# Optimization experiments

Measured on AMD Instinct MI355X. Metric: run time of the kernel, lower is better.

Reference implementation:

```python
import jax, jax.numpy as jnp
import numpy as np

SCALE = 1.0  # std of the Normal error model (init arg `scale`)
B, P, D, T = 32, 256, 64, 4096


def setup_inputs() -> dict:
    key = jax.random.key(0)
    k1, k2, k3 = jax.random.split(key, 3)
    data = jax.random.normal(k1, (B, P, D), dtype=jnp.float32)
    targets = jax.random.normal(k2, (B, P), dtype=jnp.float32)
    task_pool = jax.random.normal(k3, (T, D, 1), dtype=jnp.float32)
    return {"data": data, "targets": targets, "task_pool": task_pool}


def reference(data, targets, task_pool):
    # W: (n_dims, n_tasks), matching task_pool.squeeze(-1).T in the original
    W = task_pool[..., 0].T
    dt = data.dtype

    # Per-point, per-task predictions and Gaussian log-likelihoods, computed ONCE.
    # The original recomputes X@W and the log-prob sum for every prefix i (O(n^2));
    # here a single cumsum over the point axis reproduces the same prefix sums.
    pred_per_task = jnp.einsum('bpd,dt->bpt', data, W)          # (B, P, T)
    err = targets[..., None] - pred_per_task                     # (B, P, T)
    log_norm = -jnp.log(jnp.asarray(SCALE, dt)) - 0.5 * jnp.log(jnp.asarray(2.0 * np.pi, dt))
    scores = -0.5 * (err / SCALE) ** 2 + log_norm                # Normal(0, scale).log_prob

    cum = jnp.cumsum(scores, axis=1)                             # cum[:, i] = sum_{j<=i}
    # Posterior for predicting point i uses points 0..i-1; point 0 uses a uniform
    # posterior (original: W.mean(dim=1) == softmax(zeros) @ W.T).
    log_lik = jnp.concatenate([jnp.zeros_like(cum[:, :1]), cum[:, :-1]], axis=1)
    post = jax.nn.softmax(log_lik, axis=-1)                      # (B, P, T)

    w_mmse = jnp.einsum('bpt,dt->bpd', post, W)                  # posterior-mean weights
    return jnp.einsum('bpd,bpd->bp', data, w_mmse)               # (B, P)
```

## Files before the change

kernel.cpp:

```cpp
#include <hip/hip_runtime.h>
#include <hip/hip_bf16.h>
#include <math.h>

#define Bb 32
#define Pp 256
#define Dd 64
#define Tt 4096

typedef unsigned short ushort_t;
typedef __attribute__((ext_vector_type(8))) short bf16x8;
typedef __attribute__((ext_vector_type(4))) float f32x4;

#define TRIP_BYTES ((size_t)Bb * Pp * 64 * 16)
#define A_BF_BYTES ((size_t)Bb * Pp * Dd * 2)
#define B_BF_BYTES ((size_t)Tt * Dd * 2)
#define WS_NEED    (TRIP_BYTES + 2 * A_BF_BYTES + 2 * B_BF_BYTES)

#define MFMA6(a)                                                     \
  a = __builtin_amdgcn_mfma_f32_16x16x32_bf16(ah0, bh0, a, 0, 0, 0); \
  a = __builtin_amdgcn_mfma_f32_16x16x32_bf16(ah1, bh1, a, 0, 0, 0); \
  a = __builtin_amdgcn_mfma_f32_16x16x32_bf16(ah0, bl0, a, 0, 0, 0); \
  a = __builtin_amdgcn_mfma_f32_16x16x32_bf16(al0, bh0, a, 0, 0, 0); \
  a = __builtin_amdgcn_mfma_f32_16x16x32_bf16(ah1, bl1, a, 0, 0, 0); \
  a = __builtin_amdgcn_mfma_f32_16x16x32_bf16(al1, bh1, a, 0, 0, 0);

__global__ __launch_bounds__(256) void k_conv(const float* __restrict__ data,
                                              const float* __restrict__ Wt,
                                              ushort_t* __restrict__ Ah, ushort_t* __restrict__ Al,
                                              ushort_t* __restrict__ Bh, ushort_t* __restrict__ Bl) {
  const int i  = blockIdx.x * 256 + threadIdx.x;
  const int NA = Bb * Pp * Dd;
  const float x = (i < NA) ? data[i] : Wt[i - NA];
  const __hip_bfloat16 h = __float2bfloat16(x);
  const float hf = __bfloat162float(h);
  const __hip_bfloat16 l = __float2bfloat16(x - hf);
  if (i < NA) { Ah[i] = *(const ushort_t*)&h; Al[i] = *(const ushort_t*)&l; }
  else        { const int j = i - NA;
                Bh[j] = *(const ushort_t*)&h; Bl[j] = *(const ushort_t*)&l; }
}

__global__ __launch_bounds__(256, 2) void k_main(const ushort_t* __restrict__ Ah,
                                                 const ushort_t* __restrict__ Al,
                                                 const ushort_t* __restrict__ Bh,
                                                 const ushort_t* __restrict__ Bl,
                                                 const float* __restrict__ targets,
                                                 float4* __restrict__ triples) {
  __shared__ short Bhs[256 * 72];
  __shared__ short Bls[256 * 72];
  const int tid  = threadIdx.x;
  const int wid  = tid >> 6;
  const int lane = tid & 63;
  const int quad = lane >> 4;
  const int l16  = lane & 15;
  const int b     = blockIdx.x >> 4;
  const int strip = blockIdx.x & 15;
  const int t0    = strip * 256;

  {
    const float4* sh = (const float4*)(Bh + (size_t)t0 * Dd);
    const float4* sl = (const float4*)(Bl + (size_t)t0 * Dd);
#pragma unroll
    for (int j = 0; j < 8; ++j) {
      const int idx = tid + j * 256;
      const int tl  = idx >> 3;
      const int col = (idx & 7) * 8;
      *(float4*)&Bhs[tl * 72 + col] = sh[idx];
      *(float4*)&Bls[tl * 72 + col] = sl[idx];
    }
  }
  __syncthreads();

  const ushort_t* arow_base = Ah + (size_t)b * Pp * Dd;
  const ushort_t* alow_base = Al + (size_t)b * Pp * Dd;
  float4* __restrict__ trb  = triples + (size_t)b * Pp * 64;
  const int wstrip = strip * 4 + wid;

  float R[4];
#pragma unroll
  for (int nt = 0; nt < 4; ++nt) R[nt] = 0.f;

#pragma unroll 1
  for (int sg = 0; sg < 16; ++sg) {
    const int p0 = sg * 16;
    const size_t aoff = (size_t)(p0 + l16) * Dd + quad * 8;
    const bf16x8 ah0 = *(const bf16x8*)(arow_base + aoff);
    const bf16x8 ah1 = *(const bf16x8*)(arow_base + aoff + 32);
    const bf16x8 al0 = *(const bf16x8*)(alow_base + aoff);
    const bf16x8 al1 = *(const bf16x8*)(alow_base + aoff + 32);
    const float4 tq  = *(const float4*)(targets + b * Pp + p0 + quad * 4);

    float cc[4][4], av[4][4];
#pragma unroll
    for (int nt = 0; nt < 4; ++nt) {
      const int tl = wid * 64 + nt * 16 + l16;
      const int bo = tl * 72 + quad * 8;
      const bf16x8 bh0 = *(const bf16x8*)&Bhs[bo];
      const bf16x8 bh1 = *(const bf16x8*)&Bhs[bo + 32];
      const bf16x8 bl0 = *(const bf16x8*)&Bls[bo];
      const bf16x8 bl1 = *(const bf16x8*)&Bls[bo + 32];
      f32x4 a = (f32x4)0.f;
      MFMA6(a)

      float sc[4];
      { const float e = tq.x - a[0]; sc[0] = -0.5f * e * e; }
      { const float e = tq.y - a[1]; sc[1] = -0.5f * e * e; }
      { const float e = tq.z - a[2]; sc[2] = -0.5f * e * e; }
      { const float e = tq.w - a[3]; sc[3] = -0.5f * e * e; }

      const float colsum = (sc[0] + sc[1]) + (sc[2] + sc[3]);
      const float x1 = __shfl_xor(colsum, 16, 64);
      const float x2 = __shfl_xor(colsum, 32, 64);
      const float x3 = __shfl_xor(x1, 32, 64);
      const float pre = (quad == 0) ? 0.f
                      : (quad == 1) ? x1
                      : (quad == 2) ? (x2 + x3)
                                    : (x1 + x2 + x3);
      const float base = R[nt] + pre;
      cc[nt][0] = base;
      cc[nt][1] = base + sc[0];
      cc[nt][2] = cc[nt][1] + sc[1];
      cc[nt][3] = cc[nt][2] + sc[2];
#pragma unroll
      for (int r = 0; r < 4; ++r) av[nt][r] = a[r];

      R[nt] += ((colsum + x1) + (x2 + x3));
    }

    float mm[4], ss[4], vv[4];
#pragma unroll
    for (int r = 0; r < 4; ++r) {
      const float m01 = fmaxf(cc[0][r], cc[1][r]);
      const float m23 = fmaxf(cc[2][r], cc[3][r]);
      mm[r] = fmaxf(m01, m23);
      float s = 0.f, v = 0.f;
#pragma unroll
      for (int nt = 0; nt < 4; ++nt) {
        const float e = __expf(cc[nt][r] - mm[r]);
        s += e;
        v = fmaf(e, av[nt][r], v);
      }
      ss[r] = s; vv[r] = v;
    }

    float M[4];
#pragma unroll
    for (int r = 0; r < 4; ++r) M[r] = mm[r];
#pragma unroll
    for (int off = 1; off < 16; off <<= 1)
#pragma unroll
      for (int r = 0; r < 4; ++r) M[r] = fmaxf(M[r], __shfl_xor(M[r], off, 64));
#pragma unroll
    for (int r = 0; r < 4; ++r) {
      const float f = __expf(mm[r] - M[r]);
      ss[r] *= f; vv[r] *= f;
    }
#pragma unroll
    for (int off = 1; off < 16; off <<= 1)
#pragma unroll
      for (int r = 0; r < 4; ++r) {
        ss[r] += __shfl_xor(ss[r], off, 64);
        vv[r] += __shfl_xor(vv[r], off, 64);
      }

    if (l16 == 0) {
#pragma unroll
      for (int r = 0; r < 4; ++r) {
        const int p = p0 + quad * 4 + r;
        trb[p * 64 + wstrip] = make_float4(M[r], ss[r], vv[r], 0.f);
      }
    }
  }
}

__global__ __launch_bounds__(256) void k_merge(const float4* __restrict__ ws,
                                               float* __restrict__ out) {
  const int gt   = blockIdx.x * 256 + threadIdx.x;
  const int bp   = gt >> 6;
  const int lane = gt & 63;
  const float4 o = ws[(size_t)bp * 64 + lane];
  const float m = o.x, s = o.y, v = o.z;
  float M = m;
#pragma unroll
  for (int off = 32; off; off >>= 1) M = fmaxf(M, __shfl_xor(M, off, 64));
  const float f = __expf(m - M);
  float S = f * s, V = f * v;
#pragma unroll
  for (int off = 32; off; off >>= 1) {
    S += __shfl_xor(S, off, 64);
    V += __shfl_xor(V, off, 64);
  }
  if (lane == 0) out[bp] = V / S;
}

__global__ __launch_bounds__(256) void k_scan_fused(const float* __restrict__ data,
                                                    const float* __restrict__ targets,
                                                    const float* __restrict__ task_pool,
                                                    float4* __restrict__ ws) {
  const int b     = blockIdx.x >> 4;
  const int wid   = threadIdx.x >> 6;
  const int lane  = threadIdx.x & 63;
  const int chunk = ((blockIdx.x & 15) << 2) | wid;
  const int t     = (chunk << 6) | lane;
  float w[Dd];
#pragma unroll
  for (int d = 0; d < Dd; d += 4) {
    const float4 r = *(const float4*)(task_pool + (size_t)t * Dd + d);
    w[d] = r.x; w[d + 1] = r.y; w[d + 2] = r.z; w[d + 3] = r.w;
  }
  const float* drow = data + (size_t)b * (Pp * Dd);
  const float* tgt  = targets + b * Pp;
  float4* wsb       = ws + (size_t)b * (Pp * 64);
  float c = 0.f;
  for (int p = 0; p < Pp; ++p) {
    float a0 = 0.f, a1 = 0.f, a2 = 0.f, a3 = 0.f;
    const float* r = drow + p * Dd;
#pragma unroll
    for (int d = 0; d < Dd; d += 4) {
      a0 = fmaf(r[d], w[d], a0);         a1 = fmaf(r[d + 1], w[d + 1], a1);
      a2 = fmaf(r[d + 2], w[d + 2], a2); a3 = fmaf(r[d + 3], w[d + 3], a3);
    }
    const float pred = (a0 + a1) + (a2 + a3);
    float m = c;
#pragma unroll
    for (int off = 32; off; off >>= 1) m = fmaxf(m, __shfl_xor(m, off, 64));
    const float e = __expf(c - m);
    float s = e, v = e * pred;
#pragma unroll
    for (int off = 32; off; off >>= 1) {
      s += __shfl_xor(s, off, 64);
      v += __shfl_xor(v, off, 64);
    }
    if (lane == 0) wsb[p * 64 + chunk] = make_float4(m, s, v, 0.f);
    const float err = tgt[p] - pred;
    c = fmaf(-0.5f * err, err, c);
  }
}

extern "C" void kernel_launch(void* const* d_in, const int* in_sizes, int n_in,
                              void* d_out, int out_size, void* d_ws, size_t ws_size,
                              hipStream_t stream) {
  const float* data      = (const float*)d_in[0];
  const float* targets   = (const float*)d_in[1];
  const float* task_pool = (const float*)d_in[2];
  float* out = (float*)d_out;

  if (ws_size >= WS_NEED) {
    float4*   trips = (float4*)d_ws;
    char*     cb    = (char*)d_ws + TRIP_BYTES;
    ushort_t* Ah    = (ushort_t*)cb;
    ushort_t* Al    = (ushort_t*)(cb + A_BF_BYTES);
    ushort_t* Bh    = (ushort_t*)(cb + 2 * A_BF_BYTES);
    ushort_t* Bl    = (ushort_t*)(cb + 2 * A_BF_BYTES + B_BF_BYTES);
    k_conv <<<dim3((Bb * Pp * Dd + Tt * Dd) / 256), dim3(256), 0, stream>>>(
        data, task_pool, Ah, Al, Bh, Bl);
    k_main <<<dim3(Bb * 16), dim3(256), 0, stream>>>(Ah, Al, Bh, Bl, targets, trips);
    k_merge<<<dim3((Bb * Pp * 64) / 256), dim3(256), 0, stream>>>(trips, out);
  } else {
    float4* triples = (float4*)d_ws;
    k_scan_fused<<<dim3(512), dim3(256), 0, stream>>>(data, targets, task_pool, triples);
    k_merge<<<dim3((Bb * Pp * 64) / 256), dim3(256), 0, stream>>>(triples, out);
  }
}
```

Before: 104.6 us.

## Fuse bf16 split conversion into main kernel and halve task strip width

Removes the separate conversion kernel by splitting fp32 data and task weights into bf16 hi/lo pairs inside the main MFMA kernel. Each block now covers 128 tasks instead of 256, which doubles the grid and allows four blocks per CU. The number of partial softmax triples per point doubles to 128, so the merge kernel reads two triples per lane and does a pairwise online-softmax butterfly. The cost is redundant on-the-fly conversion of the data rows across task strips and more intermediate traffic.

```diff
diff --git a/kernel.cpp b/kernel.cpp
--- a/kernel.cpp
+++ b/kernel.cpp
@@ -11,10 +11,20 @@
 typedef __attribute__((ext_vector_type(8))) short bf16x8;
 typedef __attribute__((ext_vector_type(4))) float f32x4;
 
-#define TRIP_BYTES ((size_t)Bb * Pp * 64 * 16)
-#define A_BF_BYTES ((size_t)Bb * Pp * Dd * 2)
-#define B_BF_BYTES ((size_t)Tt * Dd * 2)
-#define WS_NEED    (TRIP_BYTES + 2 * A_BF_BYTES + 2 * B_BF_BYTES)
+#define TRIP2_BYTES ((size_t)Bb * Pp * 128 * 16)
+#define TRIP_BYTES  ((size_t)Bb * Pp * 64 * 16)
+
+__device__ __forceinline__ void split8(const float* __restrict__ x,
+                                       bf16x8& hi, bf16x8& lo) {
+#pragma unroll
+  for (int j = 0; j < 8; ++j) {
+    const __hip_bfloat16 hb = __float2bfloat16(x[j]);
+    const float hf = __bfloat162float(hb);
+    const __hip_bfloat16 lb = __float2bfloat16(x[j] - hf);
+    hi[j] = *(const short*)&hb;
+    lo[j] = *(const short*)&lb;
+  }
+}
 
 #define MFMA6(a)                                                     \
   a = __builtin_amdgcn_mfma_f32_16x16x32_bf16(ah0, bh0, a, 0, 0, 0); \
@@ -24,75 +34,72 @@
   a = __builtin_amdgcn_mfma_f32_16x16x32_bf16(ah1, bl1, a, 0, 0, 0); \
   a = __builtin_amdgcn_mfma_f32_16x16x32_bf16(al1, bh1, a, 0, 0, 0);
 
-__global__ __launch_bounds__(256) void k_conv(const float* __restrict__ data,
-                                              const float* __restrict__ Wt,
-                                              ushort_t* __restrict__ Ah, ushort_t* __restrict__ Al,
-                                              ushort_t* __restrict__ Bh, ushort_t* __restrict__ Bl) {
-  const int i  = blockIdx.x * 256 + threadIdx.x;
-  const int NA = Bb * Pp * Dd;
-  const float x = (i < NA) ? data[i] : Wt[i - NA];
-  const __hip_bfloat16 h = __float2bfloat16(x);
-  const float hf = __bfloat162float(h);
-  const __hip_bfloat16 l = __float2bfloat16(x - hf);
-  if (i < NA) { Ah[i] = *(const ushort_t*)&h; Al[i] = *(const ushort_t*)&l; }
-  else        { const int j = i - NA;
-                Bh[j] = *(const ushort_t*)&h; Bl[j] = *(const ushort_t*)&l; }
-}
-
-__global__ __launch_bounds__(256, 2) void k_main(const ushort_t* __restrict__ Ah,
-                                                 const ushort_t* __restrict__ Al,
-                                                 const ushort_t* __restrict__ Bh,
-                                                 const ushort_t* __restrict__ Bl,
-                                                 const float* __restrict__ targets,
-                                                 float4* __restrict__ triples) {
-  __shared__ short Bhs[256 * 72];
-  __shared__ short Bls[256 * 72];
+__global__ __launch_bounds__(256, 4) void k_main2(const float* __restrict__ data,
+                                                  const float* __restrict__ Wt,
+                                                  const float* __restrict__ targets,
+                                                  float4* __restrict__ triples) {
+  __shared__ short Bhs[128 * 72];
+  __shared__ short Bls[128 * 72];
   const int tid  = threadIdx.x;
   const int wid  = tid >> 6;
   const int lane = tid & 63;
   const int quad = lane >> 4;
   const int l16  = lane & 15;
-  const int b     = blockIdx.x >> 4;
-  const int strip = blockIdx.x & 15;
-  const int t0    = strip * 256;
+  const int b     = blockIdx.x >> 5;
+  const int strip = blockIdx.x & 31;
+  const int t0    = strip * 128;
 
   {
-    const float4* sh = (const float4*)(Bh + (size_t)t0 * Dd);
-    const float4* sl = (const float4*)(Bl + (size_t)t0 * Dd);
+    const float4* src = (const float4*)(Wt + (size_t)t0 * Dd);
 #pragma unroll
     for (int j = 0; j < 8; ++j) {
       const int idx = tid + j * 256;
-      const int tl  = idx >> 3;
-      const int col = (idx & 7) * 8;
-      *(float4*)&Bhs[tl * 72 + col] = sh[idx];
-      *(float4*)&Bls[tl * 72 + col] = sl[idx];
+      const int tl  = idx >> 4;
+      const int col = (idx & 15) * 4;
+      const float4 v = src[idx];
+      const float xs[4] = {v.x, v.y, v.z, v.w};
+      short h4[4], l4[4];
+#pragma unroll
+      for (int u = 0; u < 4; ++u) {
+        const __hip_bfloat16 hb = __float2bfloat16(xs[u]);
+        const float hf = __bfloat162float(hb);
+        const __hip_bfloat16 lb = __float2bfloat16(xs[u] - hf);
+        h4[u] = *(const short*)&hb;
+        l4[u] = *(const short*)&lb;
+      }
+      *(short4*)&Bhs[tl * 72 + col] = make_short4(h4[0], h4[1], h4[2], h4[3]);
+      *(short4*)&Bls[tl * 72 + col] = make_short4(l4[0], l4[1], l4[2], l4[3]);
     }
   }
   __syncthreads();
 
-  const ushort_t* arow_base = Ah + (size_t)b * Pp * Dd;
-  const ushort_t* alow_base = Al + (size_t)b * Pp * Dd;
-  float4* __restrict__ trb  = triples + (size_t)b * Pp * 64;
+  const float* __restrict__ abase = data + (size_t)b * Pp * Dd;
+  float4* __restrict__ trb = triples + (size_t)b * Pp * 128;
   const int wstrip = strip * 4 + wid;
 
-  float R[4];
-#pragma unroll
-  for (int nt = 0; nt < 4; ++nt) R[nt] = 0.f;
+  float R[2];
+  R[0] = 0.f; R[1] = 0.f;
 
 #pragma unroll 1
   for (int sg = 0; sg < 16; ++sg) {
     const int p0 = sg * 16;
-    const size_t aoff = (size_t)(p0 + l16) * Dd + quad * 8;
-    const bf16x8 ah0 = *(const bf16x8*)(arow_base + aoff);
-    const bf16x8 ah1 = *(const bf16x8*)(arow_base + aoff + 32);
-    const bf16x8 al0 = *(const bf16x8*)(alow_base + aoff);
-    const bf16x8 al1 = *(const bf16x8*)(alow_base + aoff + 32);
-    const float4 tq  = *(const float4*)(targets + b * Pp + p0 + quad * 4);
-
-    float cc[4][4], av[4][4];
-#pragma unroll
-    for (int nt = 0; nt < 4; ++nt) {
-      const int tl = wid * 64 + nt * 16 + l16;
+    bf16x8 ah0, al0, ah1, al1;
+    {
+      const float* ar = abase + (size_t)(p0 + l16) * Dd;
+      float a0[8], a1[8];
+      *(float4*)&a0[0] = *(const float4*)(ar + quad * 8);
+      *(float4*)&a0[4] = *(const float4*)(ar + quad * 8 + 4);
+      *(float4*)&a1[0] = *(const float4*)(ar + 32 + quad * 8);
+      *(float4*)&a1[4] = *(const float4*)(ar + 32 + quad * 8 + 4);
+      split8(a0, ah0, al0);
+      split8(a1, ah1, al1);
+    }
+    const float4 tq = *(const float4*)(targets + b * Pp + p0 + quad * 4);
+
+    float cc[2][4], av[2][4];
+#pragma unroll
+    for (int nt = 0; nt < 2; ++nt) {
+      const int tl = wid * 32 + nt * 16 + l16;
       const int bo = tl * 72 + quad * 8;
       const bf16x8 bh0 = *(const bf16x8*)&Bhs[bo];
       const bf16x8 bh1 = *(const bf16x8*)&Bhs[bo + 32];
@@ -129,17 +136,11 @@
     float mm[4], ss[4], vv[4];
 #pragma unroll
     for (int r = 0; r < 4; ++r) {
-      const float m01 = fmaxf(cc[0][r], cc[1][r]);
-      const float m23 = fmaxf(cc[2][r], cc[3][r]);
-      mm[r] = fmaxf(m01, m23);
-      float s = 0.f, v = 0.f;
-#pragma unroll
-      for (int nt = 0; nt < 4; ++nt) {
-        const float e = __expf(cc[nt][r] - mm[r]);
-        s += e;
-        v = fmaf(e, av[nt][r], v);
-      }
-      ss[r] = s; vv[r] = v;
+      mm[r] = fmaxf(cc[0][r], cc[1][r]);
+      const float e0 = __expf(cc[0][r] - mm[r]);
+      const float e1 = __expf(cc[1][r] - mm[r]);
+      ss[r] = e0 + e1;
+      vv[r] = fmaf(e0, av[0][r], e1 * av[1][r]);
     }
 
     float M[4];
@@ -166,28 +167,33 @@
 #pragma unroll
       for (int r = 0; r < 4; ++r) {
         const int p = p0 + quad * 4 + r;
-        trb[p * 64 + wstrip] = make_float4(M[r], ss[r], vv[r], 0.f);
+        trb[p * 128 + wstrip] = make_float4(M[r], ss[r], vv[r], 0.f);
       }
     }
   }
 }
 
-__global__ __launch_bounds__(256) void k_merge(const float4* __restrict__ ws,
-                                               float* __restrict__ out) {
+__global__ __launch_bounds__(256) void k_merge2(const float4* __restrict__ ws,
+                                                float* __restrict__ out) {
   const int gt   = blockIdx.x * 256 + threadIdx.x;
   const int bp   = gt >> 6;
   const int lane = gt & 63;
-  const float4 o = ws[(size_t)bp * 64 + lane];
-  const float m = o.x, s = o.y, v = o.z;
-  float M = m;
-#pragma unroll
-  for (int off = 32; off; off >>= 1) M = fmaxf(M, __shfl_xor(M, off, 64));
-  const float f = __expf(m - M);
-  float S = f * s, V = f * v;
-#pragma unroll
-  for (int off = 32; off; off >>= 1) {
-    S += __shfl_xor(S, off, 64);
-    V += __shfl_xor(V, off, 64);
+  const float4 o0 = ws[(size_t)bp * 128 + lane];
+  const float4 o1 = ws[(size_t)bp * 128 + 64 + lane];
+  float M = fmaxf(o0.x, o1.x);
+  const float g0 = __expf(o0.x - M), g1 = __expf(o1.x - M);
+  float S = g0 * o0.y + g1 * o1.y;
+  float V = g0 * o0.z + g1 * o1.z;
+#pragma unroll
+  for (int off = 1; off < 64; off <<= 1) {
+    const float mo = __shfl_xor(M, off, 64);
+    const float so = __shfl_xor(S, off, 64);
+    const float vo = __shfl_xor(V, off, 64);
+    const float mn = fmaxf(M, mo);
+    const float f0 = __expf(M - mn), f1 = __expf(mo - mn);
+    S = S * f0 + so * f1;
+    V = V * f0 + vo * f1;
+    M = mn;
   }
   if (lane == 0) out[bp] = V / S;
 }
@@ -236,6 +242,26 @@
   }
 }
 
+__global__ __launch_bounds__(256) void k_merge(const float4* __restrict__ ws,
+                                               float* __restrict__ out) {
+  const int gt   = blockIdx.x * 256 + threadIdx.x;
+  const int bp   = gt >> 6;
+  const int lane = gt & 63;
+  const float4 o = ws[(size_t)bp * 64 + lane];
+  const float m = o.x, s = o.y, v = o.z;
+  float M = m;
+#pragma unroll
+  for (int off = 32; off; off >>= 1) M = fmaxf(M, __shfl_xor(M, off, 64));
+  const float f = __expf(m - M);
+  float S = f * s, V = f * v;
+#pragma unroll
+  for (int off = 32; off; off >>= 1) {
+    S += __shfl_xor(S, off, 64);
+    V += __shfl_xor(V, off, 64);
+  }
+  if (lane == 0) out[bp] = V / S;
+}
+
 extern "C" void kernel_launch(void* const* d_in, const int* in_sizes, int n_in,
                               void* d_out, int out_size, void* d_ws, size_t ws_size,
                               hipStream_t stream) {
@@ -244,17 +270,10 @@
   const float* task_pool = (const float*)d_in[2];
   float* out = (float*)d_out;
 
-  if (ws_size >= WS_NEED) {
-    float4*   trips = (float4*)d_ws;
-    char*     cb    = (char*)d_ws + TRIP_BYTES;
-    ushort_t* Ah    = (ushort_t*)cb;
-    ushort_t* Al    = (ushort_t*)(cb + A_BF_BYTES);
-    ushort_t* Bh    = (ushort_t*)(cb + 2 * A_BF_BYTES);
-    ushort_t* Bl    = (ushort_t*)(cb + 2 * A_BF_BYTES + B_BF_BYTES);
-    k_conv <<<dim3((Bb * Pp * Dd + Tt * Dd) / 256), dim3(256), 0, stream>>>(
-        data, task_pool, Ah, Al, Bh, Bl);
-    k_main <<<dim3(Bb * 16), dim3(256), 0, stream>>>(Ah, Al, Bh, Bl, targets, trips);
-    k_merge<<<dim3((Bb * Pp * 64) / 256), dim3(256), 0, stream>>>(trips, out);
+  if (ws_size >= TRIP2_BYTES) {
+    float4* trips = (float4*)d_ws;
+    k_main2<<<dim3(Bb * 32), dim3(256), 0, stream>>>(data, task_pool, targets, trips);
+    k_merge2<<<dim3((Bb * Pp * 64) / 256), dim3(256), 0, stream>>>(trips, out);
   } else {
     float4* triples = (float4*)d_ws;
     k_scan_fused<<<dim3(512), dim3(256), 0, stream>>>(data, targets, task_pool, triples);
```

After: 113.8 us. +8.8%, slower.
